# Kernel tuning notes

Hardware: AMD Instinct MI355X
Metric: run time of the kernel (lower is better)

Reference implementation:

```python
import jax, jax.numpy as jnp
import numpy as np

KA = 2  # kernel_att == stride

def _unfold2(t):
    # torch nn.Unfold(kernel=2, stride=2, pad=0): [B,C,H,W] -> [B, C, 4, L], L=(H/2)*(W/2)
    B, C, H, W = t.shape
    t = t.reshape(B, C, H // KA, KA, W // KA, KA).transpose(0, 1, 3, 5, 2, 4)
    return t.reshape(B, C, KA * KA, (H // KA) * (W // KA))

def _fold2(t, H, W):
    # inverse of _unfold2 (non-overlapping): [B, C, 4, L] -> [B, C, H, W]
    B, C, _, L = t.shape
    t = t.reshape(B, C, KA, KA, H // KA, W // KA).transpose(0, 1, 4, 2, 5, 3)
    return t.reshape(B, C, H, W)

def setup_inputs() -> dict:
    key = jax.random.key(0)
    ks = jax.random.split(key, 5)
    b, c, m, h, w = 4, 16, 8, 64, 64
    O = 64
    return {
        "x": jax.random.normal(ks[0], (b, c, m, h, w), jnp.float32),
        "w_q": jax.random.normal(ks[1], (O, m), jnp.float32) * 0.1,
        "w_k": jax.random.normal(ks[2], (O, m), jnp.float32) * 0.1,
        "w_v": jax.random.normal(ks[3], (O, m), jnp.float32) * 0.1,
        "w_p": jax.random.normal(ks[4], (2,), jnp.float32) * 0.1,
    }

def reference(x, w_q, w_k, w_v, w_p):
    b, c, m, h, w = x.shape
    O = w_q.shape[0]
    # res = AdaptiveAvgPool3d((1, dim, dim)) with h==w==dim -> mean over m only
    res = x.mean(axis=2, keepdims=True)            # [b, c, 1, h, w]
    xf = x.reshape(b * c, m, h, w)
    # 1x1 convs (bias-free) are channel matmuls
    q = jnp.einsum('om,bmhw->bohw', w_q, xf)       # [b*c, O, h, w]
    k = jnp.einsum('om,bmhw->bohw', w_k, xf)
    v = jnp.einsum('om,bmhw->bohw', w_v, xf)
    # relative position map pe = conv_p(position(h, w)) -> [1,1,h,w]
    loc_w = jnp.linspace(-1.0, 1.0, w)[None, :]    # varies along W
    loc_h = jnp.linspace(-1.0, 1.0, h)[:, None]    # varies along H
    pe = (w_p[0] * loc_w + w_p[1] * loc_h)[None, None]  # [1,1,h,w]
    q5 = q.reshape(b, c, O, h, w).transpose(0, 2, 1, 3, 4)  # permuted: [b, O, c, h, w]
    k5 = k.reshape(b, c, O, h, w) + pe             # pe broadcast over trailing (h,w)
    v5 = v.reshape(b, c, O, h, w)
    scaling = float(h) ** (-0.5)
    B = b * O
    q_att = (q5 * scaling).reshape(B, c, h, w)
    # NB: torch code views the UNpermuted [b,c,O,h,w] buffer as [b*O, c, h, w] (raw reinterpretation)
    k_att = k5.reshape(B, c, h, w)
    v_att = v5.reshape(B, c, h, w)
    uq = _unfold2(q_att)                           # [B, c, 4, L]
    uk = _unfold2(k_att) + _unfold2(pe)            # unfold_rpe broadcast: [B, c, 4, L]
    uv = _unfold2(v_att)
    # att[B,i,j,l] = sum_p q[B,i,p,l] * k[B,j,p,l]
    att = jnp.einsum('bipl,bjpl->bijl', uq, uk)    # [B, c, c, L]
    att = jax.nn.softmax(att, axis=2)
    out = jnp.einsum('bijl,bjpl->bipl', att, uv)   # [B, c, 4, L]
    out = _fold2(out, h, w)                        # [B, c, h, w]
    out = out.reshape(b, O, c, h, w).transpose(0, 2, 1, 3, 4)  # [b, c, O, h, w]
    return out + res
```

## Files before the change

### kernel.cpp

```cpp
#include <hip/hip_runtime.h>

typedef unsigned int u32;
typedef float v2f __attribute__((ext_vector_type(2)));


__global__ __launch_bounds__(256, 1) void adapt_attn(
    const float* __restrict__ x,  const float* __restrict__ wq,
    const float* __restrict__ wk, const float* __restrict__ wv,
    const float* __restrict__ wp, float* __restrict__ out)
{
    __shared__ __align__(16) float s_wk[128];
    __shared__ __align__(16) float s_wv[128];
    __shared__ float s_wq[8];

    const int tid = threadIdx.x;
    const int bid = blockIdx.x;
    const int bb    = bid >> 8;
    const int o     = (bid >> 2) & 63;
    const int patch = ((bid & 3) << 8) + tid;
    const int r   = o & 3;
    const int qch = o >> 2;

    if (tid < 128) {
        s_wk[tid] = wk[(r << 7) + tid];
        s_wv[tid] = wv[(r << 7) + tid];
    } else if (tid < 136) {
        s_wq[tid - 128] = 0.125f * wq[(o << 3) + (tid - 128)];
    }
    __syncthreads();

    const int hh = patch >> 5, ww = patch & 31;
    const int y0 = hh << 1;

    const float wp0 = wp[0];
    const float wp1 = wp[1];
    const float step = 2.0f / 63.0f;
    const float lx0 = -1.0f + step * (float)(ww << 1);
    const float lx1 = lx0 + step;
    const float ly0 = -1.0f + step * (float)y0;
    const float ly1 = ly0 + step;
    v2f pea = { 2.0f * (wp0 * lx0 + wp1 * ly0), 2.0f * (wp0 * lx1 + wp1 * ly0) };
    v2f peb = { 2.0f * (wp0 * lx0 + wp1 * ly1), 2.0f * (wp0 * lx1 + wp1 * ly1) };

    const v2f* __restrict__ x2 = (const v2f*)x;
    const int sp_off = y0 * 32 + ww;

    v2f xa[8], xb[8];
    {
        const int basek = ((bb << 4) + qch) * 16384 + sp_off;
        #pragma unroll
        for (int m = 0; m < 8; m++) {
            xa[m] = x2[basek + m * 2048];
            xb[m] = x2[basek + m * 2048 + 32];
        }
    }

    v2f uka[16], ukb[16], uva[16], uvb[16];
    const float4* wk4 = (const float4*)s_wk;
    const float4* wv4 = (const float4*)s_wv;
    #pragma unroll
    for (int j = 0; j < 16; j++) {
        const float4 w0 = wk4[j * 2], w1 = wk4[j * 2 + 1];
        const float4 c0 = wv4[j * 2], c1 = wv4[j * 2 + 1];
        v2f ka = pea, kb = peb;
        v2f va = {0.f, 0.f}, vb = {0.f, 0.f};
        ka += xa[0] * w0.x; kb += xb[0] * w0.x; va += xa[0] * c0.x; vb += xb[0] * c0.x;
        ka += xa[1] * w0.y; kb += xb[1] * w0.y; va += xa[1] * c0.y; vb += xb[1] * c0.y;
        ka += xa[2] * w0.z; kb += xb[2] * w0.z; va += xa[2] * c0.z; vb += xb[2] * c0.z;
        ka += xa[3] * w0.w; kb += xb[3] * w0.w; va += xa[3] * c0.w; vb += xb[3] * c0.w;
        ka += xa[4] * w1.x; kb += xb[4] * w1.x; va += xa[4] * c1.x; vb += xb[4] * c1.x;
        ka += xa[5] * w1.y; kb += xb[5] * w1.y; va += xa[5] * c1.y; vb += xb[5] * c1.y;
        ka += xa[6] * w1.z; kb += xb[6] * w1.z; va += xa[6] * c1.z; vb += xb[6] * c1.z;
        ka += xa[7] * w1.w; kb += xb[7] * w1.w; va += xa[7] * c1.w; vb += xb[7] * c1.w;
        uka[j] = ka; ukb[j] = kb; uva[j] = va; uvb[j] = vb;
    }

    float wqr[8];
    #pragma unroll
    for (int m = 0; m < 8; m++) wqr[m] = s_wq[m];

    v2f* __restrict__ out2 = (v2f*)out;
    const int baseq0 = (bb << 4) * 16384 + sp_off;
    const int obase0 = ((bb << 4) * 64 + o) * 2048 + sp_off;

    #pragma unroll 1
    for (int i = 0; i < 16; i++) {
        const int bq = baseq0 + i * 16384;
        v2f qa[8], qb[8];
        #pragma unroll
        for (int m = 0; m < 8; m++) {
            qa[m] = x2[bq + m * 2048];
            qb[m] = x2[bq + m * 2048 + 32];
        }
        v2f uqa = {0.f, 0.f}, uqb = {0.f, 0.f};
        v2f rsa = {0.f, 0.f}, rsb = {0.f, 0.f};
        #pragma unroll
        for (int m = 0; m < 8; m++) {
            uqa += qa[m] * wqr[m];
            uqb += qb[m] * wqr[m];
            rsa += qa[m];
            rsb += qb[m];
        }

        float att[16];
        float sum = 0.f;
        #pragma unroll
        for (int j = 0; j < 16; j++) {
            v2f t = uqa * uka[j];
            t += uqb * ukb[j];
            const float e = __expf(t.x + t.y);
            att[j] = e;
            sum += e;
        }
        const float rcp = 1.0f / sum;

        v2f oa = {0.f, 0.f}, ob = {0.f, 0.f};
        #pragma unroll
        for (int j = 0; j < 16; j++) {
            oa += uva[j] * att[j];
            ob += uvb[j] * att[j];
        }
        oa = oa * rcp + rsa * 0.125f;
        ob = ob * rcp + rsb * 0.125f;

        const int obi = obase0 + i * 131072;
        out2[obi]      = oa;
        out2[obi + 32] = ob;
    }
}

extern "C" void kernel_launch(void* const* d_in, const int* in_sizes, int n_in,
                              void* d_out, int out_size, void* d_ws, size_t ws_size,
                              hipStream_t stream) {
    const float* x  = (const float*)d_in[0];
    const float* wq = (const float*)d_in[1];
    const float* wk = (const float*)d_in[2];
    const float* wv = (const float*)d_in[3];
    const float* wp = (const float*)d_in[4];
    float* out = (float*)d_out;
    adapt_attn<<<dim3(1024), dim3(256), 0, stream>>>(x, wq, wk, wv, wp, out);
}
```

Baseline: 123.1 us.

## Split per-patch query loop across threads, sharing K/V projections through LDS

Each block now handles a 16-patch tile for one (batch, O) pair. The 16 query channels are spread across thread groups instead of being looped over serially in one thread. The K and V projections are computed cooperatively once per tile and stored in shared memory, which removes the large per-thread register arrays. The grid grows 16x and launch bounds now allow higher occupancy, so more waves are available to hide the latency of the global x loads. The cost is extra LDS traffic and two barriers per block.

Measured after the change: 125.0 us. About the same (+1.6%).

```diff
diff --git a/kernel.cpp b/kernel.cpp
--- a/kernel.cpp
+++ b/kernel.cpp
@@ -1,25 +1,28 @@
 #include <hip/hip_runtime.h>
 
-typedef unsigned int u32;
 typedef float v2f __attribute__((ext_vector_type(2)));
 
 
-__global__ __launch_bounds__(256, 1) void adapt_attn(
+__global__ __launch_bounds__(256, 6) void adapt_attn(
     const float* __restrict__ x,  const float* __restrict__ wq,
     const float* __restrict__ wk, const float* __restrict__ wv,
     const float* __restrict__ wp, float* __restrict__ out)
 {
     __shared__ __align__(16) float s_wk[128];
     __shared__ __align__(16) float s_wv[128];
-    __shared__ float s_wq[8];
+    __shared__ float  s_wq[8];
+    __shared__ v2f    s_xk[8][2][16];
+    __shared__ float4 s_uk[16][16];
+    __shared__ float4 s_uv[16][16];
 
     const int tid = threadIdx.x;
     const int bid = blockIdx.x;
-    const int bb    = bid >> 8;
-    const int o     = (bid >> 2) & 63;
-    const int patch = ((bid & 3) << 8) + tid;
-    const int r   = o & 3;
-    const int qch = o >> 2;
+    const int tile = bid & 63;
+    const int o    = (bid >> 6) & 63;
+    const int bb   = bid >> 12;
+    const int r = o & 3, qch = o >> 2;
+    const int y0  = (tile >> 1) << 1;
+    const int ww0 = (tile & 1) << 4;
 
     if (tid < 128) {
         s_wk[tid] = wk[(r << 7) + tid];
@@ -27,73 +30,61 @@
     } else if (tid < 136) {
         s_wq[tid - 128] = 0.125f * wq[(o << 3) + (tid - 128)];
     }
+
+    const v2f* __restrict__ x2 = (const v2f*)x;
+
+    {
+        const int p = tid & 15, row = (tid >> 4) & 1, m = tid >> 5;
+        const int g = ((bb << 4) + qch) * 16384 + m * 2048 + (y0 + row) * 32 + ww0 + p;
+        s_xk[m][row][p] = x2[g];
+    }
     __syncthreads();
 
-    const int hh = patch >> 5, ww = patch & 31;
-    const int y0 = hh << 1;
+    {
+        const int p = tid & 15, j = tid >> 4;
+        const float wp0 = wp[0], wp1 = wp[1];
+        const float step = 2.0f / 63.0f;
+        const int wwp = ww0 + p;
+        const float lx0 = -1.0f + step * (float)(wwp << 1);
+        const float lx1 = lx0 + step;
+        const float ly0 = -1.0f + step * (float)y0;
+        const float ly1 = ly0 + step;
+        v2f ka = { 2.0f * (wp0 * lx0 + wp1 * ly0), 2.0f * (wp0 * lx1 + wp1 * ly0) };
+        v2f kb = { 2.0f * (wp0 * lx0 + wp1 * ly1), 2.0f * (wp0 * lx1 + wp1 * ly1) };
+        v2f va = {0.f, 0.f}, vb = {0.f, 0.f};
 
-    const float wp0 = wp[0];
-    const float wp1 = wp[1];
-    const float step = 2.0f / 63.0f;
-    const float lx0 = -1.0f + step * (float)(ww << 1);
-    const float lx1 = lx0 + step;
-    const float ly0 = -1.0f + step * (float)y0;
-    const float ly1 = ly0 + step;
-    v2f pea = { 2.0f * (wp0 * lx0 + wp1 * ly0), 2.0f * (wp0 * lx1 + wp1 * ly0) };
-    v2f peb = { 2.0f * (wp0 * lx0 + wp1 * ly1), 2.0f * (wp0 * lx1 + wp1 * ly1) };
+        float wkj[8], wvj[8];
+        *(float4*)&wkj[0] = ((const float4*)s_wk)[j * 2];
+        *(float4*)&wkj[4] = ((const float4*)s_wk)[j * 2 + 1];
+        *(float4*)&wvj[0] = ((const float4*)s_wv)[j * 2];
+        *(float4*)&wvj[4] = ((const float4*)s_wv)[j * 2 + 1];
 
-    const v2f* __restrict__ x2 = (const v2f*)x;
-    const int sp_off = y0 * 32 + ww;
-
-    v2f xa[8], xb[8];
-    {
-        const int basek = ((bb << 4) + qch) * 16384 + sp_off;
         #pragma unroll
         for (int m = 0; m < 8; m++) {
-            xa[m] = x2[basek + m * 2048];
-            xb[m] = x2[basek + m * 2048 + 32];
+            const v2f xa = s_xk[m][0][p];
+            const v2f xb = s_xk[m][1][p];
+            ka += xa * wkj[m]; kb += xb * wkj[m];
+            va += xa * wvj[m]; vb += xb * wvj[m];
         }
+        s_uk[j][p] = make_float4(ka.x, ka.y, kb.x, kb.y);
+        s_uv[j][p] = make_float4(va.x, va.y, vb.x, vb.y);
     }
+    __syncthreads();
 
-    v2f uka[16], ukb[16], uva[16], uvb[16];
-    const float4* wk4 = (const float4*)s_wk;
-    const float4* wv4 = (const float4*)s_wv;
-    #pragma unroll
-    for (int j = 0; j < 16; j++) {
-        const float4 w0 = wk4[j * 2], w1 = wk4[j * 2 + 1];
-        const float4 c0 = wv4[j * 2], c1 = wv4[j * 2 + 1];
-        v2f ka = pea, kb = peb;
-        v2f va = {0.f, 0.f}, vb = {0.f, 0.f};
-        ka += xa[0] * w0.x; kb += xb[0] * w0.x; va += xa[0] * c0.x; vb += xb[0] * c0.x;
-        ka += xa[1] * w0.y; kb += xb[1] * w0.y; va += xa[1] * c0.y; vb += xb[1] * c0.y;
-        ka += xa[2] * w0.z; kb += xb[2] * w0.z; va += xa[2] * c0.z; vb += xb[2] * c0.z;
-        ka += xa[3] * w0.w; kb += xb[3] * w0.w; va += xa[3] * c0.w; vb += xb[3] * c0.w;
-        ka += xa[4] * w1.x; kb += xb[4] * w1.x; va += xa[4] * c1.x; vb += xb[4] * c1.x;
-        ka += xa[5] * w1.y; kb += xb[5] * w1.y; va += xa[5] * c1.y; vb += xb[5] * c1.y;
-        ka += xa[6] * w1.z; kb += xb[6] * w1.z; va += xa[6] * c1.z; vb += xb[6] * c1.z;
-        ka += xa[7] * w1.w; kb += xb[7] * w1.w; va += xa[7] * c1.w; vb += xb[7] * c1.w;
-        uka[j] = ka; ukb[j] = kb; uva[j] = va; uvb[j] = vb;
-    }
+    {
+        const int p = tid & 15, i = tid >> 4;
+        float wqr[8];
+        #pragma unroll
+        for (int m = 0; m < 8; m++) wqr[m] = s_wq[m];
 
-    float wqr[8];
-    #pragma unroll
-    for (int m = 0; m < 8; m++) wqr[m] = s_wq[m];
-
-    v2f* __restrict__ out2 = (v2f*)out;
-    const int baseq0 = (bb << 4) * 16384 + sp_off;
-    const int obase0 = ((bb << 4) * 64 + o) * 2048 + sp_off;
-
-    #pragma unroll 1
-    for (int i = 0; i < 16; i++) {
-        const int bq = baseq0 + i * 16384;
+        const int bq = ((bb << 4) + i) * 16384 + y0 * 32 + ww0 + p;
         v2f qa[8], qb[8];
         #pragma unroll
         for (int m = 0; m < 8; m++) {
             qa[m] = x2[bq + m * 2048];
             qb[m] = x2[bq + m * 2048 + 32];
         }
-        v2f uqa = {0.f, 0.f}, uqb = {0.f, 0.f};
-        v2f rsa = {0.f, 0.f}, rsb = {0.f, 0.f};
+        v2f uqa = {0.f,0.f}, uqb = {0.f,0.f}, rsa = {0.f,0.f}, rsb = {0.f,0.f};
         #pragma unroll
         for (int m = 0; m < 8; m++) {
             uqa += qa[m] * wqr[m];
@@ -106,24 +97,27 @@
         float sum = 0.f;
         #pragma unroll
         for (int j = 0; j < 16; j++) {
-            v2f t = uqa * uka[j];
-            t += uqb * ukb[j];
+            const float4 k4 = s_uk[j][p];
+            v2f t = uqa * (v2f){k4.x, k4.y};
+            t += uqb * (v2f){k4.z, k4.w};
             const float e = __expf(t.x + t.y);
             att[j] = e;
             sum += e;
         }
         const float rcp = 1.0f / sum;
 
-        v2f oa = {0.f, 0.f}, ob = {0.f, 0.f};
+        v2f oa = {0.f,0.f}, ob = {0.f,0.f};
         #pragma unroll
         for (int j = 0; j < 16; j++) {
-            oa += uva[j] * att[j];
-            ob += uvb[j] * att[j];
+            const float4 v4 = s_uv[j][p];
+            oa += (v2f){v4.x, v4.y} * att[j];
+            ob += (v2f){v4.z, v4.w} * att[j];
         }
         oa = oa * rcp + rsa * 0.125f;
         ob = ob * rcp + rsb * 0.125f;
 
-        const int obi = obase0 + i * 131072;
+        v2f* __restrict__ out2 = (v2f*)out;
+        const int obi = (((bb << 4) + i) * 64 + o) * 2048 + y0 * 32 + ww0 + p;
         out2[obi]      = oa;
         out2[obi + 32] = ob;
     }
@@ -138,5 +132,5 @@
     const float* wv = (const float*)d_in[3];
     const float* wp = (const float*)d_in[4];
     float* out = (float*)d_out;
-    adapt_attn<<<dim3(1024), dim3(256), 0, stream>>>(x, wq, wk, wv, wp, out);
+    adapt_attn<<<dim3(16384), dim3(256), 0, stream>>>(x, wq, wk, wv, wp, out);
 }
```
